# Kernel tuning notes

Hardware: AMD Instinct MI355X
Metric: run time of the kernel (lower is better)

## Reference

```python
import jax, jax.numpy as jnp
import numpy as np
from jax import lax

N = 50000       # nodes
E = 1600000     # edges
D_IN = 1024     # input feature size
H = 256         # hidden size
L = 64          # GCN2Conv layers
C = 4           # n_classes
ALPHA = 0.2
THETA = 0.5


def setup_inputs() -> dict:
    key = jax.random.key(0)
    ks = jax.random.split(key, 7)
    x = jax.random.normal(ks[0], (N, D_IN), dtype=jnp.float32)
    edge_index = jax.random.randint(ks[1], (2, E), 0, N, dtype=jnp.int32)
    proj_W = jax.random.normal(ks[2], (D_IN, H), dtype=jnp.float32) * 0.02
    proj_b = jnp.zeros((H,), dtype=jnp.float32)
    weights = jax.random.normal(ks[3], (L, H, H), dtype=jnp.float32) * 0.05
    cls_W = jax.random.normal(ks[4], (H, C), dtype=jnp.float32) * 0.05
    cls_b = jnp.zeros((C,), dtype=jnp.float32)
    return {"x": x, "edge_index": edge_index, "proj_W": proj_W,
            "proj_b": proj_b, "weights": weights, "cls_W": cls_W, "cls_b": cls_b}


def reference(x, edge_index, proj_W, proj_b, weights, cls_W, cls_b):
    # Dropout is identity in eval mode (reference baseline).
    src, dst = edge_index[0], edge_index[1]
    # gcn_norm with added self-loops: A_hat = D^{-1/2} (A + I) D^{-1/2}
    loops = jnp.arange(N, dtype=src.dtype)
    src_f = jnp.concatenate([src, loops])
    dst_f = jnp.concatenate([dst, loops])
    deg = jax.ops.segment_sum(jnp.ones((E + N,), jnp.float32), dst_f, num_segments=N)
    dinv = jnp.where(deg > 0, lax.rsqrt(deg), 0.0)
    norm = dinv[src_f] * dinv[dst_f]  # [E+N]

    h0 = x @ proj_W + proj_b          # project: [N, H]
    betas = jnp.log(THETA / jnp.arange(1, L + 1, dtype=jnp.float32) + 1.0)  # [L]

    def step(h, wb):
        W, beta = wb
        # propagate: out[i] = sum_{(j->i)} norm * h[j]
        agg = jax.ops.segment_sum(norm[:, None] * h[src_f], dst_f, num_segments=N)
        s = (1.0 - ALPHA) * agg + ALPHA * h0     # initial residual
        h = (1.0 - beta) * s + beta * (s @ W)    # identity mapping (shared weights)
        return jax.nn.relu(h), None

    h, _ = lax.scan(step, h0, (weights, betas))
    out = h @ cls_W + cls_b  # classifier: [N, C]
    return out
```

## Files before the change

kernel.cpp:

```cpp
#include <hip/hip_runtime.h>
#include <math.h>

#define N_NODES 50000
#define N_EDGES 1600000
#define DIN 1024
#define H 256
#define L_LAYERS 64
#define ALPHA 0.2f
#define NCHUNK 8
#define CCOLS 32
#define EW_CAP (N_EDGES + 4 * N_NODES)
#define SPMM_BLOCKS 2048
#define BLK_PER_CHUNK (SPMM_BLOCKS / NCHUNK)

typedef unsigned short u16;
typedef short short8 __attribute__((ext_vector_type(8)));
typedef unsigned short ushort8_t __attribute__((ext_vector_type(8)));
typedef float f32x4 __attribute__((ext_vector_type(4)));
typedef float f32x2 __attribute__((ext_vector_type(2)));
typedef unsigned int u32x4 __attribute__((ext_vector_type(4)));

__device__ inline float b2f(u16 h) { return __uint_as_float(((unsigned)h) << 16); }
__device__ inline u16 f2b(float f) {
  unsigned u = __float_as_uint(f);
  unsigned r = u + 0x7FFFu + ((u >> 16) & 1u);
  return (u16)(r >> 16);
}

__device__ inline f32x2 bp2f(unsigned u) {
  f32x2 p;
  p[0] = __uint_as_float(u << 16);
  p[1] = __uint_as_float(u & 0xFFFF0000u);
  return p;
}

__device__ inline size_t bidx(int node, int col) {
  return ((size_t)(col >> 5) * N_NODES + node) * CCOLS + (col & 31);
}

__global__ void GCNIIForDialog_18923625906417_kernel() {}

__global__ __launch_bounds__(256) void k_zero(int* __restrict__ p, int n) {
  int i = blockIdx.x * 256 + threadIdx.x;
  if (i < n) p[i] = 0;
}

__global__ __launch_bounds__(256) void k_count(const int* __restrict__ dst, int* __restrict__ cnt) {
  int e = blockIdx.x * 256 + threadIdx.x;
  if (e < N_EDGES) atomicAdd(&cnt[dst[e]], 1);
}

__global__ __launch_bounds__(256) void k_dinv(const int* __restrict__ cnt, float* __restrict__ dinv) {
  int i = blockIdx.x * 256 + threadIdx.x;
  if (i < N_NODES) dinv[i] = 1.0f / sqrtf((float)(cnt[i] + 1));
}

__global__ __launch_bounds__(1024) void k_scan(const int* __restrict__ cnt, int* __restrict__ offs) {
  const int CH = (N_NODES + 1023) / 1024;
  __shared__ int sums[1024];
  int t = threadIdx.x;
  int lo = t * CH, hi = lo + CH;
  if (hi > N_NODES) hi = N_NODES;
  int s = 0;
  for (int i = lo; i < hi; ++i) s += (cnt[i] + 3) & ~3;
  sums[t] = s;
  __syncthreads();
  for (int d = 1; d < 1024; d <<= 1) {
    int v = (t >= d) ? sums[t - d] : 0;
    __syncthreads();
    sums[t] += v;
    __syncthreads();
  }
  int run = (t == 0) ? 0 : sums[t - 1];
  for (int i = lo; i < hi; ++i) { offs[i] = run; run += (cnt[i] + 3) & ~3; }
  if (t == 0) offs[N_NODES] = sums[1023];
}

__global__ __launch_bounds__(256) void k_scatter(const int* __restrict__ src, const int* __restrict__ dst,
    const int* __restrict__ offs, int* __restrict__ cursor, const float* __restrict__ dinv,
    unsigned* __restrict__ ew) {
  int e = blockIdx.x * 256 + threadIdx.x;
  if (e >= N_EDGES) return;
  int sN = src[e], dN = dst[e];
  int pos = offs[dN] + atomicAdd(&cursor[dN], 1);
  unsigned wb = (unsigned)f2b(dinv[sN] * dinv[dN]);
  ew[pos] = (wb << 16) | (unsigned)sN;
}

__global__ void k_wtr(const float* __restrict__ Win, u16* __restrict__ Wout) {
  __shared__ float tile[32][33];
  size_t base = (size_t)blockIdx.z * H * H;
  int n0 = blockIdx.x * 32, k0 = blockIdx.y * 32;
  for (int i = threadIdx.y; i < 32; i += 8)
    tile[i][threadIdx.x] = Win[base + (size_t)(k0 + i) * H + n0 + threadIdx.x];
  __syncthreads();
  for (int i = threadIdx.y; i < 32; i += 8)
    Wout[base + (size_t)(n0 + i) * H + k0 + threadIdx.x] = f2b(tile[threadIdx.x][i]);
}

__global__ void k_trP(const float* __restrict__ Win, u16* __restrict__ Wout) {
  __shared__ float tile[32][33];
  int n0 = blockIdx.x * 32, k0 = blockIdx.y * 32;
  for (int i = threadIdx.y; i < 32; i += 8)
    tile[i][threadIdx.x] = Win[(size_t)(k0 + i) * H + n0 + threadIdx.x];
  __syncthreads();
  for (int i = threadIdx.y; i < 32; i += 8)
    Wout[(size_t)(n0 + i) * DIN + k0 + threadIdx.x] = f2b(tile[threadIdx.x][i]);
}

__global__ __launch_bounds__(256) void k_spmm(
    const u16* __restrict__ hb, const u16* __restrict__ h0b,
    const int* __restrict__ offs, const unsigned* __restrict__ ew,
    const float* __restrict__ dinv, u16* __restrict__ sbb)
{
  const int NBLK = (N_NODES + 15) / 16;
  int chunk = blockIdx.x & 7;
  int bslot = blockIdx.x >> 3;
  int wid = threadIdx.x >> 6, lane = threadIdx.x & 63;
  int sub = lane & 3;
  int eslot = (lane >> 2) & 3;
  int nsub = lane >> 4;
  const u16* hc = hb + (size_t)chunk * N_NODES * CCOLS;
  const u16* hp = hc + sub * 8;

  for (int nb = bslot; nb < NBLK; nb += BLK_PER_CHUNK) {
    int node = nb * 16 + wid * 4 + nsub;
    if (node >= N_NODES) continue;
    f32x2 acc2[4] = {};
    int i0 = offs[node], end = offs[node + 1];
    for (int i = i0 + eslot * 4; i < end; i += 16) {
      u32x4 er = __builtin_nontemporal_load((const u32x4*)(ew + i));
      u32x4 v0 = *(const u32x4*)(hp + (size_t)(er[0] & 0xFFFFu) * CCOLS);
      u32x4 v1 = *(const u32x4*)(hp + (size_t)(er[1] & 0xFFFFu) * CCOLS);
      u32x4 v2 = *(const u32x4*)(hp + (size_t)(er[2] & 0xFFFFu) * CCOLS);
      u32x4 v3 = *(const u32x4*)(hp + (size_t)(er[3] & 0xFFFFu) * CCOLS);
      float w0 = __uint_as_float(er[0] & 0xFFFF0000u);
      float w1 = __uint_as_float(er[1] & 0xFFFF0000u);
      float w2 = __uint_as_float(er[2] & 0xFFFF0000u);
      float w3 = __uint_as_float(er[3] & 0xFFFF0000u);
      f32x2 w0v = {w0, w0}, w1v = {w1, w1}, w2v = {w2, w2}, w3v = {w3, w3};
#pragma unroll
      for (int j = 0; j < 4; ++j) acc2[j] += w0v * bp2f(v0[j]);
#pragma unroll
      for (int j = 0; j < 4; ++j) acc2[j] += w1v * bp2f(v1[j]);
#pragma unroll
      for (int j = 0; j < 4; ++j) acc2[j] += w2v * bp2f(v2[j]);
#pragma unroll
      for (int j = 0; j < 4; ++j) acc2[j] += w3v * bp2f(v3[j]);
    }
#pragma unroll
    for (int d = 4; d <= 8; d <<= 1)
#pragma unroll
      for (int j = 0; j < 4; ++j) {
        acc2[j][0] += __shfl_xor(acc2[j][0], d);
        acc2[j][1] += __shfl_xor(acc2[j][1], d);
      }
    if (eslot == 0) {
      float di = dinv[node];
      float di2 = di * di;
      size_t ci = (size_t)chunk * N_NODES * CCOLS + (size_t)node * CCOLS + sub * 8;
      ushort8_t hv = *(const ushort8_t*)(hp + (size_t)node * CCOLS);
      ushort8_t h0v = __builtin_nontemporal_load((const ushort8_t*)(h0b + ci));
      ushort8_t o;
#pragma unroll
      for (int j = 0; j < 4; ++j) {
#pragma unroll
        for (int c = 0; c < 2; ++c) {
          int k = 2 * j + c;
          float v = (1.0f - ALPHA) * (acc2[j][c] + di2 * b2f(hv[k])) + ALPHA * b2f(h0v[k]);
          o[k] = f2b(v);
        }
      }
      __builtin_nontemporal_store(o, (ushort8_t*)(sbb + ci));
    }
  }
}

__global__ __launch_bounds__(256) void k_gemm(
    const u16* __restrict__ A, const u16* __restrict__ BT,
    u16* __restrict__ Hout, float beta)
{
  __shared__ u16 As[128 * 40];
  __shared__ u16 Bs[128 * 40];
  int tid = threadIdx.x;
  int mBase = blockIdx.x * 128, nBase = blockIdx.y * 128;
  int wid = tid >> 6, lane = tid & 63;
  int wm = (wid & 1) * 64, wn = (wid >> 1) * 64;
  int lrow = lane & 15, quad = lane >> 4;
  f32x4 acc[4][4] = {};
  int sr = tid >> 2, sc = tid & 3;
  for (int k0 = 0; k0 < H; k0 += 32) {
    const u16* Ac = A + (size_t)(k0 >> 5) * N_NODES * CCOLS;
#pragma unroll
    for (int it = 0; it < 2; ++it) {
      int r = sr + it * 64;
      int grow = mBase + r;
      u32x4 va = {};
      if (grow < N_NODES) va = *(const u32x4*)(Ac + (size_t)grow * CCOLS + sc * 8);
      *(u32x4*)&As[r * 40 + sc * 8] = va;
      u32x4 vb = *(const u32x4*)(BT + (size_t)(nBase + r) * H + k0 + sc * 8);
      *(u32x4*)&Bs[r * 40 + sc * 8] = vb;
    }
    __syncthreads();
    short8 af[4], bfr[4];
#pragma unroll
    for (int i = 0; i < 4; ++i) {
      af[i]  = *(const short8*)&As[(wm + i * 16 + lrow) * 40 + quad * 8];
      bfr[i] = *(const short8*)&Bs[(wn + i * 16 + lrow) * 40 + quad * 8];
    }
#pragma unroll
    for (int mi = 0; mi < 4; ++mi)
#pragma unroll
      for (int ni = 0; ni < 4; ++ni)
        acc[mi][ni] = __builtin_amdgcn_mfma_f32_16x16x32_bf16(af[mi], bfr[ni], acc[mi][ni], 0, 0, 0);
    __syncthreads();
  }
#pragma unroll
  for (int mi = 0; mi < 4; ++mi)
#pragma unroll
    for (int ni = 0; ni < 4; ++ni)
#pragma unroll
      for (int rg = 0; rg < 4; ++rg) {
        int r = mBase + wm + mi * 16 + quad * 4 + rg;
        int c = nBase + wn + ni * 16 + lrow;
        if (r < N_NODES) {
          size_t idx = bidx(r, c);
          float v = (1.0f - beta) * b2f(A[idx]) + beta * acc[mi][ni][rg];
          Hout[idx] = f2b(fmaxf(v, 0.0f));
        }
      }
}

__global__ __launch_bounds__(256) void k_pgemm(
    const float* __restrict__ X, const u16* __restrict__ BT,
    const float* __restrict__ bias, u16* __restrict__ h0b, u16* __restrict__ h)
{
  __shared__ u16 As[128 * 40];
  __shared__ u16 Bs[128 * 40];
  int tid = threadIdx.x;
  int mBase = blockIdx.x * 128, nBase = blockIdx.y * 128;
  int wid = tid >> 6, lane = tid & 63;
  int wm = (wid & 1) * 64, wn = (wid >> 1) * 64;
  int lrow = lane & 15, quad = lane >> 4;
  f32x4 acc[4][4] = {};
  int sr = tid >> 2, sc = tid & 3;
  for (int k0 = 0; k0 < DIN; k0 += 32) {
#pragma unroll
    for (int it = 0; it < 2; ++it) {
      int r = sr + it * 64;
      int grow = mBase + r;
      float4 fa0 = make_float4(0.f, 0.f, 0.f, 0.f);
      float4 fa1 = make_float4(0.f, 0.f, 0.f, 0.f);
      if (grow < N_NODES) {
        const float* ap = X + (size_t)grow * DIN + k0 + sc * 8;
        fa0 = *(const float4*)ap;
        fa1 = *(const float4*)(ap + 4);
      }
      ushort8_t av;
      av[0] = f2b(fa0.x); av[1] = f2b(fa0.y); av[2] = f2b(fa0.z); av[3] = f2b(fa0.w);
      av[4] = f2b(fa1.x); av[5] = f2b(fa1.y); av[6] = f2b(fa1.z); av[7] = f2b(fa1.w);
      *(ushort8_t*)&As[r * 40 + sc * 8] = av;
      u32x4 vb = *(const u32x4*)(BT + (size_t)(nBase + r) * DIN + k0 + sc * 8);
      *(u32x4*)&Bs[r * 40 + sc * 8] = vb;
    }
    __syncthreads();
    short8 af[4], bfr[4];
#pragma unroll
    for (int i = 0; i < 4; ++i) {
      af[i]  = *(const short8*)&As[(wm + i * 16 + lrow) * 40 + quad * 8];
      bfr[i] = *(const short8*)&Bs[(wn + i * 16 + lrow) * 40 + quad * 8];
    }
#pragma unroll
    for (int mi = 0; mi < 4; ++mi)
#pragma unroll
      for (int ni = 0; ni < 4; ++ni)
        acc[mi][ni] = __builtin_amdgcn_mfma_f32_16x16x32_bf16(af[mi], bfr[ni], acc[mi][ni], 0, 0, 0);
    __syncthreads();
  }
#pragma unroll
  for (int mi = 0; mi < 4; ++mi)
#pragma unroll
    for (int ni = 0; ni < 4; ++ni)
#pragma unroll
      for (int rg = 0; rg < 4; ++rg) {
        int r = mBase + wm + mi * 16 + quad * 4 + rg;
        int c = nBase + wn + ni * 16 + lrow;
        if (r < N_NODES) {
          size_t idx = bidx(r, c);
          float v = acc[mi][ni][rg] + bias[c];
          u16 bv = f2b(v);
          h0b[idx] = bv;
          h[idx] = bv;
        }
      }
}

__global__ __launch_bounds__(256) void k_cls(const u16* __restrict__ h,
    const float* __restrict__ W, const float* __restrict__ b, float* __restrict__ out)
{
  int wid = threadIdx.x >> 6, lane = threadIdx.x & 63;
  int node = blockIdx.x * 4 + wid;
  if (node >= N_NODES) return;
  float a0 = 0, a1 = 0, a2 = 0, a3 = 0;
  for (int t = lane; t < H; t += 64) {
    float hv = b2f(h[bidx(node, t)]);
    a0 += hv * W[t * 4 + 0];
    a1 += hv * W[t * 4 + 1];
    a2 += hv * W[t * 4 + 2];
    a3 += hv * W[t * 4 + 3];
  }
#pragma unroll
  for (int off = 32; off > 0; off >>= 1) {
    a0 += __shfl_down(a0, off);
    a1 += __shfl_down(a1, off);
    a2 += __shfl_down(a2, off);
    a3 += __shfl_down(a3, off);
  }
  if (lane == 0) {
    float4 o;
    o.x = a0 + b[0];
    o.y = a1 + b[1];
    o.z = a2 + b[2];
    o.w = a3 + b[3];
    *(float4*)(out + (size_t)node * 4) = o;
  }
}

extern "C" void kernel_launch(void* const* d_in, const int* in_sizes, int n_in,
                              void* d_out, int out_size, void* d_ws, size_t ws_size,
                              hipStream_t stream) {
  (void)in_sizes; (void)n_in; (void)out_size; (void)ws_size;
  const float* x     = (const float*)d_in[0];
  const int*   ei    = (const int*)d_in[1];
  const float* projW = (const float*)d_in[2];
  const float* projB = (const float*)d_in[3];
  const float* wts   = (const float*)d_in[4];
  const float* clsW  = (const float*)d_in[5];
  const float* clsB  = (const float*)d_in[6];
  float* out = (float*)d_out;

  char* ws = (char*)d_ws;
  size_t off = 0;
  auto alloc = [&](size_t bytes) -> void* {
    void* p = ws + off;
    off = (off + bytes + 255) & ~(size_t)255;
    return p;
  };
  int*   cntcur = (int*)alloc((size_t)N_NODES * 2 * 4);
  int*   cnt    = cntcur;
  int*   cursor = cntcur + N_NODES;
  int*   offs   = (int*)alloc((size_t)(N_NODES + 1) * 4);
  float* dinv   = (float*)alloc((size_t)N_NODES * 4);
  unsigned* ew  = (unsigned*)alloc((size_t)EW_CAP * 4);
  u16*   WT     = (u16*)alloc((size_t)L_LAYERS * H * H * 2);
  u16*   BTp    = (u16*)alloc((size_t)H * DIN * 2);
  u16*   h0b    = (u16*)alloc((size_t)N_NODES * H * 2);
  u16*   sb     = (u16*)alloc((size_t)N_NODES * H * 2);
  u16*   h      = (u16*)alloc((size_t)N_NODES * H * 2);

  const int* src = ei;
  const int* dst = ei + N_EDGES;

  k_zero<<<(N_NODES * 2 + 255) / 256, 256, 0, stream>>>(cntcur, N_NODES * 2);
  k_zero<<<(EW_CAP + 255) / 256, 256, 0, stream>>>((int*)ew, EW_CAP);
  k_count<<<(N_EDGES + 255) / 256, 256, 0, stream>>>(dst, cnt);
  k_dinv<<<(N_NODES + 255) / 256, 256, 0, stream>>>(cnt, dinv);
  k_scan<<<1, 1024, 0, stream>>>(cnt, offs);
  k_scatter<<<(N_EDGES + 255) / 256, 256, 0, stream>>>(src, dst, offs, cursor, dinv, ew);
  k_wtr<<<dim3(H / 32, H / 32, L_LAYERS), dim3(32, 8), 0, stream>>>(wts, WT);
  k_trP<<<dim3(H / 32, DIN / 32), dim3(32, 8), 0, stream>>>(projW, BTp);

  k_pgemm<<<dim3((N_NODES + 127) / 128, H / 128), 256, 0, stream>>>(x, BTp, projB, h0b, h);

  dim3 ggrid((N_NODES + 127) / 128, H / 128);
  for (int l = 0; l < L_LAYERS; ++l) {
    k_spmm<<<SPMM_BLOCKS, 256, 0, stream>>>(h, h0b, offs, ew, dinv, sb);
    float beta = logf(0.5f / (float)(l + 1) + 1.0f);
    k_gemm<<<ggrid, 256, 0, stream>>>(sb, WT + (size_t)l * H * H, h, beta);
  }
  k_cls<<<(N_NODES + 3) / 4, 256, 0, stream>>>(h, clsW, clsB, out);
}
```

Measured before the change: 11.52 ms.

## Use XCC-aware dynamic work claiming in SpMM propagation kernel

Replaces the static blockIdx-based chunk/node assignment in the SpMM with atomic work-stealing queues, one per column chunk per layer. Each block reads its XCC id from a hardware register and starts on the matching chunk, so a chunk's gathered rows tend to stay in one XCC's L2, then steals from the other chunks. This targets load imbalance from the varying node degrees and L2 locality across XCDs. The cost is per-claim atomics and two block barriers, and the edge-record load is no longer nontemporal.

Result: slower. 20.95 ms (+81.8%).

```diff
diff --git a/kernel.cpp b/kernel.cpp
--- a/kernel.cpp
+++ b/kernel.cpp
@@ -11,7 +11,8 @@
 #define CCOLS 32
 #define EW_CAP (N_EDGES + 4 * N_NODES)
 #define SPMM_BLOCKS 2048
-#define BLK_PER_CHUNK (SPMM_BLOCKS / NCHUNK)
+#define GRAIN 128
+#define NCLAIM ((N_NODES + GRAIN - 1) / GRAIN)
 
 typedef unsigned short u16;
 typedef short short8 __attribute__((ext_vector_type(8)));
@@ -111,67 +112,80 @@
 __global__ __launch_bounds__(256) void k_spmm(
     const u16* __restrict__ hb, const u16* __restrict__ h0b,
     const int* __restrict__ offs, const unsigned* __restrict__ ew,
-    const float* __restrict__ dinv, u16* __restrict__ sbb)
+    const float* __restrict__ dinv, u16* __restrict__ sbb,
+    int* __restrict__ work)
 {
-  const int NBLK = (N_NODES + 15) / 16;
-  int chunk = blockIdx.x & 7;
-  int bslot = blockIdx.x >> 3;
+  __shared__ int s_claim;
+  unsigned xcc = __builtin_amdgcn_s_getreg(20 | (31 << 11));
+  int mychunk = (int)(xcc & 7);
   int wid = threadIdx.x >> 6, lane = threadIdx.x & 63;
   int sub = lane & 3;
   int eslot = (lane >> 2) & 3;
   int nsub = lane >> 4;
-  const u16* hc = hb + (size_t)chunk * N_NODES * CCOLS;
-  const u16* hp = hc + sub * 8;
-
-  for (int nb = bslot; nb < NBLK; nb += BLK_PER_CHUNK) {
-    int node = nb * 16 + wid * 4 + nsub;
-    if (node >= N_NODES) continue;
-    f32x2 acc2[4] = {};
-    int i0 = offs[node], end = offs[node + 1];
-    for (int i = i0 + eslot * 4; i < end; i += 16) {
-      u32x4 er = __builtin_nontemporal_load((const u32x4*)(ew + i));
-      u32x4 v0 = *(const u32x4*)(hp + (size_t)(er[0] & 0xFFFFu) * CCOLS);
-      u32x4 v1 = *(const u32x4*)(hp + (size_t)(er[1] & 0xFFFFu) * CCOLS);
-      u32x4 v2 = *(const u32x4*)(hp + (size_t)(er[2] & 0xFFFFu) * CCOLS);
-      u32x4 v3 = *(const u32x4*)(hp + (size_t)(er[3] & 0xFFFFu) * CCOLS);
-      float w0 = __uint_as_float(er[0] & 0xFFFF0000u);
-      float w1 = __uint_as_float(er[1] & 0xFFFF0000u);
-      float w2 = __uint_as_float(er[2] & 0xFFFF0000u);
-      float w3 = __uint_as_float(er[3] & 0xFFFF0000u);
-      f32x2 w0v = {w0, w0}, w1v = {w1, w1}, w2v = {w2, w2}, w3v = {w3, w3};
-#pragma unroll
-      for (int j = 0; j < 4; ++j) acc2[j] += w0v * bp2f(v0[j]);
-#pragma unroll
-      for (int j = 0; j < 4; ++j) acc2[j] += w1v * bp2f(v1[j]);
-#pragma unroll
-      for (int j = 0; j < 4; ++j) acc2[j] += w2v * bp2f(v2[j]);
-#pragma unroll
-      for (int j = 0; j < 4; ++j) acc2[j] += w3v * bp2f(v3[j]);
-    }
-#pragma unroll
-    for (int d = 4; d <= 8; d <<= 1)
-#pragma unroll
-      for (int j = 0; j < 4; ++j) {
-        acc2[j][0] += __shfl_xor(acc2[j][0], d);
-        acc2[j][1] += __shfl_xor(acc2[j][1], d);
-      }
-    if (eslot == 0) {
-      float di = dinv[node];
-      float di2 = di * di;
-      size_t ci = (size_t)chunk * N_NODES * CCOLS + (size_t)node * CCOLS + sub * 8;
-      ushort8_t hv = *(const ushort8_t*)(hp + (size_t)node * CCOLS);
-      ushort8_t h0v = __builtin_nontemporal_load((const ushort8_t*)(h0b + ci));
-      ushort8_t o;
-#pragma unroll
-      for (int j = 0; j < 4; ++j) {
-#pragma unroll
-        for (int c = 0; c < 2; ++c) {
-          int k = 2 * j + c;
-          float v = (1.0f - ALPHA) * (acc2[j][c] + di2 * b2f(hv[k])) + ALPHA * b2f(h0v[k]);
-          o[k] = f2b(v);
+
+  for (int ci = 0; ci < NCHUNK; ++ci) {
+    int chunk = (mychunk + ci) & 7;
+    const u16* hc = hb + (size_t)chunk * N_NODES * CCOLS;
+    const u16* hp = hc + sub * 8;
+    for (;;) {
+      if (threadIdx.x == 0) s_claim = atomicAdd(&work[chunk], 1);
+      __syncthreads();
+      int claim = s_claim;
+      __syncthreads();
+      if (claim >= NCLAIM) break;
+      int base = claim * GRAIN + wid * 32 + nsub;
+#pragma unroll 1
+      for (int it = 0; it < 8; ++it) {
+        int node = base + it * 4;
+        if (node >= N_NODES) break;
+        f32x2 acc2[4] = {};
+        int i0 = offs[node], end = offs[node + 1];
+        for (int i = i0 + eslot * 4; i < end; i += 16) {
+          u32x4 er = *(const u32x4*)(ew + i);
+          u32x4 v0 = *(const u32x4*)(hp + (size_t)(er[0] & 0xFFFFu) * CCOLS);
+          u32x4 v1 = *(const u32x4*)(hp + (size_t)(er[1] & 0xFFFFu) * CCOLS);
+          u32x4 v2 = *(const u32x4*)(hp + (size_t)(er[2] & 0xFFFFu) * CCOLS);
+          u32x4 v3 = *(const u32x4*)(hp + (size_t)(er[3] & 0xFFFFu) * CCOLS);
+          float w0 = __uint_as_float(er[0] & 0xFFFF0000u);
+          float w1 = __uint_as_float(er[1] & 0xFFFF0000u);
+          float w2 = __uint_as_float(er[2] & 0xFFFF0000u);
+          float w3 = __uint_as_float(er[3] & 0xFFFF0000u);
+          f32x2 w0v = {w0, w0}, w1v = {w1, w1}, w2v = {w2, w2}, w3v = {w3, w3};
+#pragma unroll
+          for (int j = 0; j < 4; ++j) acc2[j] += w0v * bp2f(v0[j]);
+#pragma unroll
+          for (int j = 0; j < 4; ++j) acc2[j] += w1v * bp2f(v1[j]);
+#pragma unroll
+          for (int j = 0; j < 4; ++j) acc2[j] += w2v * bp2f(v2[j]);
+#pragma unroll
+          for (int j = 0; j < 4; ++j) acc2[j] += w3v * bp2f(v3[j]);
+        }
+#pragma unroll
+        for (int d = 4; d <= 8; d <<= 1)
+#pragma unroll
+          for (int j = 0; j < 4; ++j) {
+            acc2[j][0] += __shfl_xor(acc2[j][0], d);
+            acc2[j][1] += __shfl_xor(acc2[j][1], d);
+          }
+        if (eslot == 0) {
+          float di = dinv[node];
+          float di2 = di * di;
+          size_t ci2 = (size_t)chunk * N_NODES * CCOLS + (size_t)node * CCOLS + sub * 8;
+          ushort8_t hv = *(const ushort8_t*)(hp + (size_t)node * CCOLS);
+          ushort8_t h0v = __builtin_nontemporal_load((const ushort8_t*)(h0b + ci2));
+          ushort8_t o;
+#pragma unroll
+          for (int j = 0; j < 4; ++j) {
+#pragma unroll
+            for (int c = 0; c < 2; ++c) {
+              int k = 2 * j + c;
+              float v = (1.0f - ALPHA) * (acc2[j][c] + di2 * b2f(hv[k])) + ALPHA * b2f(h0v[k]);
+              o[k] = f2b(v);
+            }
+          }
+          __builtin_nontemporal_store(o, (ushort8_t*)(sbb + ci2));
         }
       }
-      __builtin_nontemporal_store(o, (ushort8_t*)(sbb + ci));
     }
   }
 }
@@ -352,6 +366,7 @@
   int*   offs   = (int*)alloc((size_t)(N_NODES + 1) * 4);
   float* dinv   = (float*)alloc((size_t)N_NODES * 4);
   unsigned* ew  = (unsigned*)alloc((size_t)EW_CAP * 4);
+  int*   work   = (int*)alloc((size_t)L_LAYERS * NCHUNK * 4);
   u16*   WT     = (u16*)alloc((size_t)L_LAYERS * H * H * 2);
   u16*   BTp    = (u16*)alloc((size_t)H * DIN * 2);
   u16*   h0b    = (u16*)alloc((size_t)N_NODES * H * 2);
@@ -363,6 +378,7 @@
 
   k_zero<<<(N_NODES * 2 + 255) / 256, 256, 0, stream>>>(cntcur, N_NODES * 2);
   k_zero<<<(EW_CAP + 255) / 256, 256, 0, stream>>>((int*)ew, EW_CAP);
+  k_zero<<<(L_LAYERS * NCHUNK + 255) / 256, 256, 0, stream>>>(work, L_LAYERS * NCHUNK);
   k_count<<<(N_EDGES + 255) / 256, 256, 0, stream>>>(dst, cnt);
   k_dinv<<<(N_NODES + 255) / 256, 256, 0, stream>>>(cnt, dinv);
   k_scan<<<1, 1024, 0, stream>>>(cnt, offs);
@@ -374,7 +390,7 @@
 
   dim3 ggrid((N_NODES + 127) / 128, H / 128);
   for (int l = 0; l < L_LAYERS; ++l) {
-    k_spmm<<<SPMM_BLOCKS, 256, 0, stream>>>(h, h0b, offs, ew, dinv, sb);
+    k_spmm<<<SPMM_BLOCKS, 256, 0, stream>>>(h, h0b, offs, ew, dinv, sb, work + l * NCHUNK);
     float beta = logf(0.5f / (float)(l + 1) + 1.0f);
     k_gemm<<<ggrid, 256, 0, stream>>>(sb, WT + (size_t)l * H * H, h, beta);
   }
```
